# Kernel optimization log

Measured on AMD Instinct MI355X. Metric: run time of the kernel, lower is better.

The kernel has to match this reference:

```python
import jax, jax.numpy as jnp
import numpy as np
import math

EMBED = 512
HEADS = 8
HEAD_DIM = EMBED // HEADS
PATCH = 4
IMG = 32
NP_SIDE = IMG // PATCH          # 8
NUM_PATCHES = NP_SIDE * NP_SIDE  # 64
SEQ = NUM_PATCHES + 1            # 65
PATCH_FEAT = PATCH * PATCH * 3   # 48
HID = 1024
NCLS = 10
B = 2048


def setup_inputs() -> dict:
    key = jax.random.key(0)
    ks = jax.random.split(key, 14)
    s = lambda fan_in: 1.0 / math.sqrt(fan_in)
    return {
        "x": jax.random.normal(ks[0], (B, 3, IMG, IMG), dtype=jnp.float32),
        "proj_w": jax.random.uniform(ks[1], (EMBED, PATCH_FEAT), minval=-s(PATCH_FEAT), maxval=s(PATCH_FEAT)),
        "proj_b": jax.random.uniform(ks[2], (EMBED,), minval=-s(PATCH_FEAT), maxval=s(PATCH_FEAT)),
        "cls": jax.random.normal(ks[3], (1, 1, EMBED), dtype=jnp.float32),
        "pos": jax.random.normal(ks[4], (SEQ, EMBED), dtype=jnp.float32),
        "wq": jax.random.uniform(ks[5], (HEADS, HEAD_DIM, EMBED), minval=-s(EMBED), maxval=s(EMBED)),
        "bq": jax.random.uniform(ks[6], (HEADS, HEAD_DIM), minval=-s(EMBED), maxval=s(EMBED)),
        "wo": jax.random.uniform(ks[7], (EMBED, EMBED), minval=-s(EMBED), maxval=s(EMBED)),
        "bo": jax.random.uniform(ks[8], (EMBED,), minval=-s(EMBED), maxval=s(EMBED)),
        "w1": jax.random.uniform(ks[9], (HID, EMBED), minval=-s(EMBED), maxval=s(EMBED)),
        "b1": jax.random.uniform(ks[10], (HID,), minval=-s(EMBED), maxval=s(EMBED)),
        "w2": jax.random.uniform(ks[11], (NCLS, HID), minval=-s(HID), maxval=s(HID)),
        "b2": jax.random.uniform(ks[12], (NCLS,), minval=-s(HID), maxval=s(HID)),
    }


def reference(x, proj_w, proj_b, cls, pos, wq, bq, wo, bo, w1, b1, w2, b2):
    b = x.shape[0]
    # nn.Unfold(kernel=4, stride=4): per-patch vector ordered (C, kh, kw)
    p = x.reshape(b, 3, NP_SIDE, PATCH, NP_SIDE, PATCH)
    p = p.transpose(0, 2, 4, 1, 3, 5).reshape(b, NUM_PATCHES, PATCH_FEAT)
    emb = p @ proj_w.T + proj_b                                   # [B, 64, 512]
    seq = jnp.concatenate([jnp.broadcast_to(cls, (b, 1, EMBED)), emb], axis=1)
    seq = seq + pos                                               # [B, 65, 512]

    # Faithful bug: q, k, v all come from the query projection
    q = jnp.einsum('bsd,hkd->bhsk', seq, wq) + bq[None, :, None, :]  # [B,H,S,Dh]
    w = jnp.einsum('bhsk,bhtk->bhst', q, q) / math.sqrt(HEAD_DIM)
    # Faithful bug: softmax over dim=1 of [B,S,S] per head -> query axis (axis=2 here)
    w = jax.nn.softmax(w, axis=2)
    att = jnp.einsum('bhst,bhtk->bhsk', w, q)                     # [B,H,S,Dh]
    mh = att.transpose(0, 2, 1, 3).reshape(b, SEQ, EMBED)
    out = mh @ wo.T + bo                                          # [B, 65, 512]

    ct = out[:, 0, :]
    h = jax.nn.gelu(ct @ w1.T + b1, approximate=False)
    logits = h @ w2.T + b2                                        # [B, 10]
    return logits
```

## Files before the change

### kernel.cpp

```cpp
#include <hip/hip_runtime.h>
#include <hip/hip_bf16.h>
#include <math.h>

#define BATCH 2048
#define SEQL 65
#define EMB 512
#define NHEADS 8
#define HD 64
#define NPATCH 64
#define PFEAT 48
#define HIDDIM 1024
#define NCLS 10

typedef short bfrag __attribute__((ext_vector_type(8)));
typedef float facc  __attribute__((ext_vector_type(16)));

union B8 { unsigned int u[4]; unsigned long long ull[2]; bfrag f; };

__device__ inline unsigned int cvt2(float a, float b) {
  __hip_bfloat162 t = __float22bfloat162_rn(float2{a, b});
  return *(unsigned int*)&t;
}
__device__ inline unsigned short f2bf(float f) {
  __hip_bfloat16 h = __float2bfloat16(f);
  return *(unsigned short*)&h;
}
__device__ inline float bf2f(unsigned short h) {
  return __uint_as_float(((unsigned int)h) << 16);
}
__device__ inline float lo16f(unsigned int u) { return __uint_as_float(u << 16); }
__device__ inline float hi16f(unsigned int u) { return __uint_as_float(u & 0xffff0000u); }
__device__ inline bfrag ldf(const unsigned short* p) {
  union { unsigned long long u[2]; bfrag s; } c;
  c.u[0] = *(const unsigned long long*)(p);
  c.u[1] = *(const unsigned long long*)(p + 4);
  return c.s;
}

__global__ __launch_bounds__(256) void k_prep(
    const float* __restrict__ wq, const float* __restrict__ proj_w,
    unsigned short* __restrict__ WcH, unsigned short* __restrict__ WcL,
    const float* __restrict__ wo, unsigned short* __restrict__ WoH,
    unsigned short* __restrict__ WoL,
    const float* __restrict__ w1, unsigned short* __restrict__ W1H,
    unsigned short* __restrict__ W1L,
    float* __restrict__ wqT)
{
  __shared__ float sm[1088];
  const int bid = blockIdx.x, tid = threadIdx.x;
  if (bid < 512) {
    float* wr = sm;
    float* part = sm + 512;
    const int hk = bid;
    wr[tid]     = wq[(size_t)hk*EMB + tid];
    wr[256+tid] = wq[(size_t)hk*EMB + 256 + tid];
    __syncthreads();
    if (tid < PFEAT*4) {
      int f = tid % PFEAT, p = tid / PFEAT;
      float a = 0.f;
      for (int d = p*128; d < (p+1)*128; ++d) a += wr[d]*proj_w[d*PFEAT + f];
      part[p*PFEAT + f] = a;
    }
    __syncthreads();
    if (tid < PFEAT) {
      float v = part[tid] + part[PFEAT+tid] + part[2*PFEAT+tid] + part[3*PFEAT+tid];
      unsigned short hi = f2bf(v);
      WcH[hk*PFEAT + tid] = hi;
      WcL[hk*PFEAT + tid] = f2bf(v - bf2f(hi));
    }
  } else if (bid < 1536) {
    int i = (bid - 512)*256 + tid;
    float v = wo[i];
    unsigned short hi = f2bf(v);
    WoH[i] = hi; WoL[i] = f2bf(v - bf2f(hi));
  } else if (bid < 3584) {
    int i = (bid - 1536)*256 + tid;
    float v = w1[i];
    unsigned short hi = f2bf(v);
    W1H[i] = hi; W1L[i] = f2bf(v - bf2f(hi));
  } else {
    float (*t)[33] = (float(*)[33])sm;
    const int r = bid - 3584, bx = (r & 15)*32, by = (r >> 4)*32;
    const int c = tid & 31, r0 = tid >> 5;
    #pragma unroll
    for (int i = 0; i < 4; ++i) {
      int rr = r0 + 8*i;
      t[rr][c] = wq[(size_t)(by + rr)*512 + bx + c];
    }
    __syncthreads();
    #pragma unroll
    for (int i = 0; i < 4; ++i) {
      int rr = r0 + 8*i;
      wqT[(size_t)(bx + rr)*512 + by + c] = t[c][rr];
    }
  }
}

__global__ __launch_bounds__(256) void k_qbias(
    const float* __restrict__ wqT, const float* __restrict__ bq,
    const float* __restrict__ cls, const float* __restrict__ pos,
    const float* __restrict__ proj_b, float* __restrict__ qbias)
{
  __shared__ float v[EMB];
  __shared__ float part[256];
  const int h = blockIdx.x / SEQL, s = blockIdx.x - h*SEQL;
  const int tid = threadIdx.x;
  const float* po = pos + (size_t)s*EMB;
  v[tid]     = po[tid]     + (s == 0 ? cls[tid]     : proj_b[tid]);
  v[256+tid] = po[256+tid] + (s == 0 ? cls[256+tid] : proj_b[256+tid]);
  __syncthreads();
  const int p = tid >> 6, k = tid & 63;
  const float* wp = wqT + h*HD + k;
  float a = 0.f;
  for (int d = p*128; d < p*128 + 128; ++d)
    a = fmaf(v[d], wp[(size_t)d*512], a);
  part[p*64 + k] = a;
  __syncthreads();
  if (tid < HD)
    qbias[((size_t)h*SEQL + s)*HD + tid] =
        part[tid] + part[64+tid] + part[128+tid] + part[192+tid] + bq[h*HD + tid];
}

__global__ __launch_bounds__(256) void k_attn(
    const float* __restrict__ x, const unsigned short* __restrict__ WcH,
    const unsigned short* __restrict__ WcL, const float* __restrict__ qbias,
    float* __restrict__ mh0)
{
  __shared__ __align__(16) char smem[19456];
  unsigned short* Qh = (unsigned short*)smem;
  float* mpart = (float*)(smem + 13056);
  float* spart = (float*)(smem + 15360);
  float* S0    = (float*)(smem + 17664);
  float* p0v   = (float*)(smem + 18048);
  float* attp  = (float*)(smem + 18432);

  const int b = blockIdx.x & 2047, h = blockIdx.x >> 11;
  const int tid = threadIdx.x, w = tid >> 6, lane = tid & 63;
  const int u2 = lane >> 5;
  const float* xb = x + (size_t)b*3072;
  const float* qb = qbias + (size_t)h*SEQL*HD;
  const float C = 0.18033688011112042f;

  {
    const int ti = w >> 1, tj = w & 1;
    const int ar = 32*ti + (lane & 31);
    const int ni = ar >> 3, nj = ar & 7;
    const float* pbase = xb + (ni*4 + 2*u2)*32 + nj*4;
    const int br = 32*tj + (lane & 31);
    const unsigned short* whp = WcH + ((size_t)(h*HD + br))*PFEAT;
    const unsigned short* wlp = WcL + ((size_t)(h*HD + br))*PFEAT;
    facc acc = {0,0,0,0,0,0,0,0,0,0,0,0,0,0,0,0};
    #pragma unroll
    for (int ks = 0; ks < 3; ++ks) {
      float4 va = *(const float4*)(pbase + ks*1024);
      float4 vb = *(const float4*)(pbase + ks*1024 + 32);
      B8 ah, al;
      ah.u[0] = cvt2(va.x, va.y); ah.u[1] = cvt2(va.z, va.w);
      ah.u[2] = cvt2(vb.x, vb.y); ah.u[3] = cvt2(vb.z, vb.w);
      al.u[0] = cvt2(va.x - lo16f(ah.u[0]), va.y - hi16f(ah.u[0]));
      al.u[1] = cvt2(va.z - lo16f(ah.u[1]), va.w - hi16f(ah.u[1]));
      al.u[2] = cvt2(vb.x - lo16f(ah.u[2]), vb.y - hi16f(ah.u[2]));
      al.u[3] = cvt2(vb.z - lo16f(ah.u[3]), vb.w - hi16f(ah.u[3]));
      const int f0 = ks*16 + u2*8;
      B8 bh, bl;
      bh.f = *(const bfrag*)(whp + f0);
      bl.f = *(const bfrag*)(wlp + f0);
      acc = __builtin_amdgcn_mfma_f32_32x32x16_bf16(ah.f, bh.f, acc, 0, 0, 0);
      acc = __builtin_amdgcn_mfma_f32_32x32x16_bf16(ah.f, bl.f, acc, 0, 0, 0);
      acc = __builtin_amdgcn_mfma_f32_32x32x16_bf16(al.f, bh.f, acc, 0, 0, 0);
    }
    #pragma unroll
    for (int r = 0; r < 16; ++r) {
      int row = (r & 3) + 8*(r >> 2) + 4*u2 + 32*ti;
      int s = 1 + row;
      Qh[s*68 + br] = f2bf(acc[r] + qb[s*HD + br]);
    }
    if (tid < HD) Qh[tid] = f2bf(qb[tid]);
    for (int i = tid; i < 31*17; i += 256) {
      int row = 65 + i/17, o = (i - (i/17)*17)*4;
      *(unsigned long long*)(Qh + row*68 + o) = 0ull;
    }
  }
  __syncthreads();

  for (int t = w; t < 9; t += 4) {
    const int ri = t/3, ci = t - ri*3;
    const int ar2 = 32*ri + (lane & 31);
    const int br2 = 32*ci + (lane & 31);
    facc a2 = {0,0,0,0,0,0,0,0,0,0,0,0,0,0,0,0};
    #pragma unroll
    for (int ks = 0; ks < 4; ++ks) {
      int k0 = ks*16 + u2*8;
      bfrag qa = ldf(Qh + ar2*68 + k0);
      bfrag qc = ldf(Qh + br2*68 + k0);
      a2 = __builtin_amdgcn_mfma_f32_32x32x16_bf16(qa, qc, a2, 0, 0, 0);
    }
    float m, s;
    if (ri == 2) {
      m = (u2 == 0) ? a2[0] : -3.0e38f;
      s = (u2 == 0) ? 1.0f : 0.0f;
    } else {
      m = a2[0];
      #pragma unroll
      for (int r = 1; r < 16; ++r) m = fmaxf(m, a2[r]);
      float mm = m * C;
      s = 0.f;
      #pragma unroll
      for (int r = 0; r < 16; ++r)
        s += __builtin_amdgcn_exp2f(fmaf(a2[r], C, -mm));
    }
    const int pi = ri*2 + u2;
    mpart[pi*96 + br2] = m;
    spart[pi*96 + br2] = s;
    if (ri == 0 && u2 == 0) S0[br2] = a2[0];
  }
  __syncthreads();

  if (tid < SEQL) {
    float m = mpart[tid];
    #pragma unroll
    for (int i = 1; i < 6; ++i) m = fmaxf(m, mpart[i*96 + tid]);
    float mm = m * C;
    float s = 0.f;
    #pragma unroll
    for (int i = 0; i < 6; ++i)
      s += spart[i*96 + tid] * __builtin_amdgcn_exp2f(fmaf(mpart[i*96 + tid], C, -mm));
    p0v[tid] = __builtin_amdgcn_exp2f(fmaf(S0[tid], C, -mm)) / s;
  }
  __syncthreads();

  {
    int k = tid & 63, p = tid >> 6;
    int t0 = p*17, t1 = (t0 + 17 < SEQL) ? t0 + 17 : SEQL;
    float a = 0.f;
    for (int t = t0; t < t1; ++t)
      a += p0v[t] * bf2f(Qh[t*68 + k]);
    attp[p*64 + k] = a;
  }
  __syncthreads();
  if (tid < HD)
    mh0[(size_t)b*EMB + h*HD + tid] =
        attp[tid] + attp[64+tid] + attp[128+tid] + attp[192+tid];
}

template<bool GELU>
__global__ __launch_bounds__(256) void k_gemm(
    const float* __restrict__ A, const unsigned short* __restrict__ WH,
    const unsigned short* __restrict__ WL, const float* __restrict__ bias,
    float* __restrict__ C, int N, int K)
{
  __shared__ __align__(16) unsigned short Ah[64*36];
  __shared__ __align__(16) unsigned short Al[64*36];
  const int tid = threadIdx.x, w = tid >> 6, lane = tid & 63;
  const int u2 = lane >> 5;
  const int m0 = blockIdx.x*64, n0 = blockIdx.y*64;
  const int ti = w >> 1, tj = w & 1;
  const int ar = 32*ti + (lane & 31);
  const int nr = n0 + 32*tj + (lane & 31);
  const unsigned short* wh = WH + (size_t)nr*K;
  const unsigned short* wl = WL + (size_t)nr*K;
  const int srow = tid >> 2, skk = (tid & 3)*8;
  const float* ap0 = A + (size_t)(m0 + srow)*K + skk;
  facc acc = {0,0,0,0,0,0,0,0,0,0,0,0,0,0,0,0};

  for (int k0 = 0; k0 < K; k0 += 32) {
    float4 a0 = *(const float4*)(ap0 + k0);
    float4 a1 = *(const float4*)(ap0 + k0 + 4);
    B8 sh, sl;
    sh.u[0] = cvt2(a0.x, a0.y); sh.u[1] = cvt2(a0.z, a0.w);
    sh.u[2] = cvt2(a1.x, a1.y); sh.u[3] = cvt2(a1.z, a1.w);
    sl.u[0] = cvt2(a0.x - lo16f(sh.u[0]), a0.y - hi16f(sh.u[0]));
    sl.u[1] = cvt2(a0.z - lo16f(sh.u[1]), a0.w - hi16f(sh.u[1]));
    sl.u[2] = cvt2(a1.x - lo16f(sh.u[2]), a1.y - hi16f(sh.u[2]));
    sl.u[3] = cvt2(a1.z - lo16f(sh.u[3]), a1.w - hi16f(sh.u[3]));
    *(unsigned long long*)(Ah + srow*36 + skk)     = sh.ull[0];
    *(unsigned long long*)(Ah + srow*36 + skk + 4) = sh.ull[1];
    *(unsigned long long*)(Al + srow*36 + skk)     = sl.ull[0];
    *(unsigned long long*)(Al + srow*36 + skk + 4) = sl.ull[1];
    __syncthreads();
    #pragma unroll
    for (int ks = 0; ks < 2; ++ks) {
      int f0 = ks*16 + u2*8;
      bfrag ah = ldf(Ah + ar*36 + f0);
      bfrag al = ldf(Al + ar*36 + f0);
      B8 bh, bl;
      bh.f = *(const bfrag*)(wh + k0 + f0);
      bl.f = *(const bfrag*)(wl + k0 + f0);
      acc = __builtin_amdgcn_mfma_f32_32x32x16_bf16(ah, bh.f, acc, 0, 0, 0);
      acc = __builtin_amdgcn_mfma_f32_32x32x16_bf16(ah, bl.f, acc, 0, 0, 0);
      acc = __builtin_amdgcn_mfma_f32_32x32x16_bf16(al, bh.f, acc, 0, 0, 0);
    }
    __syncthreads();
  }
  #pragma unroll
  for (int r = 0; r < 16; ++r) {
    int m = m0 + 32*ti + (r & 3) + 8*(r >> 2) + 4*u2;
    float c = acc[r] + bias[nr];
    if (GELU) c = 0.5f*c*(1.f + erff(c*0.70710678118654752f));
    C[(size_t)m*N + nr] = c;
  }
}

__global__ __launch_bounds__(256) void k_logits(
    const float* __restrict__ hh, const float* __restrict__ w2,
    const float* __restrict__ b2, float* __restrict__ out)
{
  const int w = threadIdx.x >> 6, lane = threadIdx.x & 63;
  const int r = blockIdx.x*4 + w;
  const float* hr = hh + (size_t)r*HIDDIM + lane*16;
  float hv[16];
  #pragma unroll
  for (int i4 = 0; i4 < 4; ++i4) {
    float4 v = *(const float4*)(hr + i4*4);
    hv[i4*4+0] = v.x; hv[i4*4+1] = v.y; hv[i4*4+2] = v.z; hv[i4*4+3] = v.w;
  }
  float acc[NCLS];
  #pragma unroll
  for (int c = 0; c < NCLS; ++c) {
    const float* wr = w2 + (size_t)c*HIDDIM + lane*16;
    float a = 0.f;
    #pragma unroll
    for (int i4 = 0; i4 < 4; ++i4) {
      float4 wv = *(const float4*)(wr + i4*4);
      a += hv[i4*4]*wv.x + hv[i4*4+1]*wv.y + hv[i4*4+2]*wv.z + hv[i4*4+3]*wv.w;
    }
    acc[c] = a;
  }
  #pragma unroll
  for (int c = 0; c < NCLS; ++c)
    #pragma unroll
    for (int m = 1; m < 64; m <<= 1) acc[c] += __shfl_xor(acc[c], m, 64);
  if (lane == 0) {
    #pragma unroll
    for (int c = 0; c < NCLS; ++c) out[(size_t)r*NCLS + c] = acc[c] + b2[c];
  }
}

extern "C" void kernel_launch(void* const* d_in, const int* in_sizes, int n_in,
                              void* d_out, int out_size, void* d_ws, size_t ws_size,
                              hipStream_t stream)
{
  const float* x      = (const float*)d_in[0];
  const float* proj_w = (const float*)d_in[1];
  const float* proj_b = (const float*)d_in[2];
  const float* cls    = (const float*)d_in[3];
  const float* pos    = (const float*)d_in[4];
  const float* wq     = (const float*)d_in[5];
  const float* bq     = (const float*)d_in[6];
  const float* wo     = (const float*)d_in[7];
  const float* bo     = (const float*)d_in[8];
  const float* w1     = (const float*)d_in[9];
  const float* b1     = (const float*)d_in[10];
  const float* w2     = (const float*)d_in[11];
  const float* b2     = (const float*)d_in[12];
  float* out = (float*)d_out;

  unsigned short* WcH = (unsigned short*)d_ws;
  unsigned short* WcL = (unsigned short*)((char*)d_ws + 49152);
  float* qbias        = (float*)((char*)d_ws + 98304);
  unsigned short* WoH = (unsigned short*)((char*)d_ws + 231424);
  unsigned short* WoL = (unsigned short*)((char*)d_ws + 755712);
  unsigned short* W1H = (unsigned short*)((char*)d_ws + 1280000);
  unsigned short* W1L = (unsigned short*)((char*)d_ws + 2328576);
  float* mh0          = (float*)((char*)d_ws + 3377152);
  float* ct           = (float*)((char*)d_ws + 7571456);
  float* hh           = (float*)((char*)d_ws + 11765760);
  float* wqT          = hh;

  hipLaunchKernelGGL(k_prep, dim3(3840), dim3(256), 0, stream,
                     wq, proj_w, WcH, WcL, wo, WoH, WoL, w1, W1H, W1L, wqT);
  hipLaunchKernelGGL(k_qbias, dim3(NHEADS*SEQL), dim3(256), 0, stream,
                     wqT, bq, cls, pos, proj_b, qbias);
  hipLaunchKernelGGL(k_attn, dim3(BATCH*NHEADS), dim3(256), 0, stream,
                     x, WcH, WcL, qbias, mh0);
  hipLaunchKernelGGL((k_gemm<false>), dim3(BATCH/64, EMB/64), dim3(256), 0, stream,
                     mh0, WoH, WoL, bo, ct, EMB, EMB);
  hipLaunchKernelGGL((k_gemm<true>),  dim3(BATCH/64, HIDDIM/64), dim3(256), 0, stream,
                     ct, W1H, W1L, b1, hh, HIDDIM, EMB);
  hipLaunchKernelGGL(k_logits, dim3(BATCH/4), dim3(256), 0, stream,
                     hh, w2, b2, out);
}
```

Before: 250.7 us.

## Pre-split GEMM activations to bf16 hi/lo and use split-K 32x32 tiles

```diff
diff --git a/kernel.cpp b/kernel.cpp
--- a/kernel.cpp
+++ b/kernel.cpp
@@ -124,7 +124,7 @@
 __global__ __launch_bounds__(256) void k_attn(
     const float* __restrict__ x, const unsigned short* __restrict__ WcH,
     const unsigned short* __restrict__ WcL, const float* __restrict__ qbias,
-    float* __restrict__ mh0)
+    unsigned short* __restrict__ mh0H, unsigned short* __restrict__ mh0L)
 {
   __shared__ __align__(16) char smem[19456];
   unsigned short* Qh = (unsigned short*)smem;
@@ -238,66 +238,61 @@
     attp[p*64 + k] = a;
   }
   __syncthreads();
-  if (tid < HD)
-    mh0[(size_t)b*EMB + h*HD + tid] =
-        attp[tid] + attp[64+tid] + attp[128+tid] + attp[192+tid];
+  if (tid < HD) {
+    float a = attp[tid] + attp[64+tid] + attp[128+tid] + attp[192+tid];
+    unsigned short hi = f2bf(a);
+    mh0H[(size_t)b*EMB + h*HD + tid] = hi;
+    mh0L[(size_t)b*EMB + h*HD + tid] = f2bf(a - bf2f(hi));
+  }
 }
 
 template<bool GELU>
 __global__ __launch_bounds__(256) void k_gemm(
-    const float* __restrict__ A, const unsigned short* __restrict__ WH,
-    const unsigned short* __restrict__ WL, const float* __restrict__ bias,
-    float* __restrict__ C, int N, int K)
-{
-  __shared__ __align__(16) unsigned short Ah[64*36];
-  __shared__ __align__(16) unsigned short Al[64*36];
+    const unsigned short* __restrict__ AH, const unsigned short* __restrict__ AL,
+    const unsigned short* __restrict__ WH, const unsigned short* __restrict__ WL,
+    const float* __restrict__ bias, float* __restrict__ Cf,
+    unsigned short* __restrict__ CH, unsigned short* __restrict__ CL,
+    int N, int K)
+{
+  __shared__ float red[4096];
   const int tid = threadIdx.x, w = tid >> 6, lane = tid & 63;
   const int u2 = lane >> 5;
-  const int m0 = blockIdx.x*64, n0 = blockIdx.y*64;
-  const int ti = w >> 1, tj = w & 1;
-  const int ar = 32*ti + (lane & 31);
-  const int nr = n0 + 32*tj + (lane & 31);
-  const unsigned short* wh = WH + (size_t)nr*K;
-  const unsigned short* wl = WL + (size_t)nr*K;
-  const int srow = tid >> 2, skk = (tid & 3)*8;
-  const float* ap0 = A + (size_t)(m0 + srow)*K + skk;
+  const int m0 = blockIdx.x*32, n0 = blockIdx.y*32;
+  const int kb = w*(K >> 2);
+  const unsigned short* ahp = AH + (size_t)(m0 + (lane & 31))*K + kb + u2*8;
+  const unsigned short* alp = AL + (size_t)(m0 + (lane & 31))*K + kb + u2*8;
+  const unsigned short* bhp = WH + (size_t)(n0 + (lane & 31))*K + kb + u2*8;
+  const unsigned short* blp = WL + (size_t)(n0 + (lane & 31))*K + kb + u2*8;
   facc acc = {0,0,0,0,0,0,0,0,0,0,0,0,0,0,0,0};
-
-  for (int k0 = 0; k0 < K; k0 += 32) {
-    float4 a0 = *(const float4*)(ap0 + k0);
-    float4 a1 = *(const float4*)(ap0 + k0 + 4);
-    B8 sh, sl;
-    sh.u[0] = cvt2(a0.x, a0.y); sh.u[1] = cvt2(a0.z, a0.w);
-    sh.u[2] = cvt2(a1.x, a1.y); sh.u[3] = cvt2(a1.z, a1.w);
-    sl.u[0] = cvt2(a0.x - lo16f(sh.u[0]), a0.y - hi16f(sh.u[0]));
-    sl.u[1] = cvt2(a0.z - lo16f(sh.u[1]), a0.w - hi16f(sh.u[1]));
-    sl.u[2] = cvt2(a1.x - lo16f(sh.u[2]), a1.y - hi16f(sh.u[2]));
-    sl.u[3] = cvt2(a1.z - lo16f(sh.u[3]), a1.w - hi16f(sh.u[3]));
-    *(unsigned long long*)(Ah + srow*36 + skk)     = sh.ull[0];
-    *(unsigned long long*)(Ah + srow*36 + skk + 4) = sh.ull[1];
-    *(unsigned long long*)(Al + srow*36 + skk)     = sl.ull[0];
-    *(unsigned long long*)(Al + srow*36 + skk + 4) = sl.ull[1];
-    __syncthreads();
-    #pragma unroll
-    for (int ks = 0; ks < 2; ++ks) {
-      int f0 = ks*16 + u2*8;
-      bfrag ah = ldf(Ah + ar*36 + f0);
-      bfrag al = ldf(Al + ar*36 + f0);
-      B8 bh, bl;
-      bh.f = *(const bfrag*)(wh + k0 + f0);
-      bl.f = *(const bfrag*)(wl + k0 + f0);
-      acc = __builtin_amdgcn_mfma_f32_32x32x16_bf16(ah, bh.f, acc, 0, 0, 0);
-      acc = __builtin_amdgcn_mfma_f32_32x32x16_bf16(ah, bl.f, acc, 0, 0, 0);
-      acc = __builtin_amdgcn_mfma_f32_32x32x16_bf16(al, bh.f, acc, 0, 0, 0);
-    }
-    __syncthreads();
-  }
-  #pragma unroll
-  for (int r = 0; r < 16; ++r) {
-    int m = m0 + 32*ti + (r & 3) + 8*(r >> 2) + 4*u2;
-    float c = acc[r] + bias[nr];
-    if (GELU) c = 0.5f*c*(1.f + erff(c*0.70710678118654752f));
-    C[(size_t)m*N + nr] = c;
+  const int kc = K >> 2;
+  for (int k = 0; k < kc; k += 16) {
+    bfrag ah = *(const bfrag*)(ahp + k);
+    bfrag al = *(const bfrag*)(alp + k);
+    bfrag bh = *(const bfrag*)(bhp + k);
+    bfrag bl = *(const bfrag*)(blp + k);
+    acc = __builtin_amdgcn_mfma_f32_32x32x16_bf16(ah, bh, acc, 0, 0, 0);
+    acc = __builtin_amdgcn_mfma_f32_32x32x16_bf16(ah, bl, acc, 0, 0, 0);
+    acc = __builtin_amdgcn_mfma_f32_32x32x16_bf16(al, bh, acc, 0, 0, 0);
+  }
+  #pragma unroll
+  for (int r = 0; r < 16; ++r) red[(w*16 + r)*64 + lane] = acc[r];
+  __syncthreads();
+  #pragma unroll
+  for (int e0 = 0; e0 < 4; ++e0) {
+    int e = e0*256 + tid;
+    int r = e >> 6, l = e & 63;
+    float c = red[e] + red[1024+e] + red[2048+e] + red[3072+e];
+    int row = m0 + (r & 3) + 8*(r >> 2) + 4*(l >> 5);
+    int col = n0 + (l & 31);
+    c += bias[col];
+    if (GELU) {
+      c = 0.5f*c*(1.f + erff(c*0.70710678118654752f));
+      Cf[(size_t)row*N + col] = c;
+    } else {
+      unsigned short hi = f2bf(c);
+      CH[(size_t)row*N + col] = hi;
+      CL[(size_t)row*N + col] = f2bf(c - bf2f(hi));
+    }
   }
 }
 
@@ -362,8 +357,10 @@
   unsigned short* WoL = (unsigned short*)((char*)d_ws + 755712);
   unsigned short* W1H = (unsigned short*)((char*)d_ws + 1280000);
   unsigned short* W1L = (unsigned short*)((char*)d_ws + 2328576);
-  float* mh0          = (float*)((char*)d_ws + 3377152);
-  float* ct           = (float*)((char*)d_ws + 7571456);
+  unsigned short* mh0H = (unsigned short*)((char*)d_ws + 3377152);
+  unsigned short* mh0L = (unsigned short*)((char*)d_ws + 5474304);
+  unsigned short* ctH  = (unsigned short*)((char*)d_ws + 7571456);
+  unsigned short* ctL  = (unsigned short*)((char*)d_ws + 9668608);
   float* hh           = (float*)((char*)d_ws + 11765760);
   float* wqT          = hh;
 
@@ -372,11 +369,12 @@
   hipLaunchKernelGGL(k_qbias, dim3(NHEADS*SEQL), dim3(256), 0, stream,
                      wqT, bq, cls, pos, proj_b, qbias);
   hipLaunchKernelGGL(k_attn, dim3(BATCH*NHEADS), dim3(256), 0, stream,
-                     x, WcH, WcL, qbias, mh0);
-  hipLaunchKernelGGL((k_gemm<false>), dim3(BATCH/64, EMB/64), dim3(256), 0, stream,
-                     mh0, WoH, WoL, bo, ct, EMB, EMB);
-  hipLaunchKernelGGL((k_gemm<true>),  dim3(BATCH/64, HIDDIM/64), dim3(256), 0, stream,
-                     ct, W1H, W1L, b1, hh, HIDDIM, EMB);
+                     x, WcH, WcL, qbias, mh0H, mh0L);
+  hipLaunchKernelGGL((k_gemm<false>), dim3(BATCH/32, EMB/32), dim3(256), 0, stream,
+                     mh0H, mh0L, WoH, WoL, bo, (float*)nullptr, ctH, ctL, EMB, EMB);
+  hipLaunchKernelGGL((k_gemm<true>),  dim3(BATCH/32, HIDDIM/32), dim3(256), 0, stream,
+                     ctH, ctL, W1H, W1L, b1, hh, (unsigned short*)nullptr,
+                     (unsigned short*)nullptr, HIDDIM, EMB);
   hipLaunchKernelGGL(k_logits, dim3(BATCH/4), dim3(256), 0, stream,
                      hh, w2, b2, out);
 }
```

Result: slower. 275.4 us (+9.8%).
